# Kernel tuning notes

Measured on AMD Instinct MI355X. Metric: run time of the kernel, lower is better.

Reference implementation:

```python
import jax, jax.numpy as jnp
import numpy as np

N, E = 20000, 5000
IN_FT, OUT_FT = 128, 128
DENSITY = 0.01  # fraction of nonzeros in the incidence matrix


def setup_inputs() -> dict:
    key = jax.random.key(0)
    kx, kh, kw, kb = jax.random.split(key, 4)
    X = jax.random.normal(kx, (N, IN_FT), dtype=jnp.float32)
    H = (jax.random.uniform(kh, (N, E)) < DENSITY).astype(jnp.float32)
    # xavier_normal_ with gain=0.01
    xav_std = 0.01 * np.sqrt(2.0 / (IN_FT + OUT_FT))
    weight_trans = jax.random.normal(kw, (IN_FT, OUT_FT), dtype=jnp.float32) * xav_std
    bias = jax.random.normal(kb, (OUT_FT,), dtype=jnp.float32) * 0.01
    return {"X": X, "H": H, "weight_trans": weight_trans, "bias": bias}


def reference(X, H, weight_trans, bias):
    # X: [N, in_ft], H: [N, E] incidence
    Xw = X @ weight_trans                      # [N, out_ft]
    DV = jnp.sum(H, axis=1) + 1e-12            # node degrees, [N]
    DE = jnp.sum(H, axis=0) + 1e-12            # hyperedge degrees, [E]
    # G = diag(1/DV) @ H @ diag(1/DE) @ H^T applied to Xw, computed in the
    # efficient order without materializing the NxN matrix G:
    M = H.T @ Xw                               # [E, out_ft]
    M = M / DE[:, None]                        # diag(1/DE) scaling
    out = H @ M                                # [N, out_ft]
    out = out / DV[:, None]                    # diag(1/DV) scaling
    out = out + bias
    return jax.nn.relu(out)
```

## Files before the change

### kernel.cpp

```cpp
#include <hip/hip_runtime.h>
#include <hip/hip_bf16.h>

typedef unsigned long long u64;

#define N_NODES 20000
#define N_EDGES 5000
#define FT 128
#define NT 20
#define NRG 313
#define ROW_U64 80
#define COL_U64 320
#define MAX_DEG 320

__global__ __launch_bounds__(256) void x_to_bf16(
    const float2* __restrict__ X2, __hip_bfloat162* __restrict__ Xb2) {
  int i = blockIdx.x * 256 + threadIdx.x;
  Xb2[i] = __float22bfloat162_rn(X2[i]);
}

__global__ __launch_bounds__(64) void scan_bitmask(
    const float4* __restrict__ H4,
    u64* __restrict__ Hbt,
    u64* __restrict__ HbtT) {
  const int lane = threadIdx.x;
  const int t  = blockIdx.x % NT;
  const int rg = blockIdx.x / NT;
  const int r0 = rg * 64;
  const int rows = min(64, N_NODES - r0);
  const int idx4 = t * 64 + lane;
  const bool lv = idx4 < 1250;

  u64 m0 = 0, m1 = 0, m2 = 0, m3 = 0;
  for (int kb = 0; kb < rows; kb += 8) {
    float4 vv[8];
#pragma unroll
    for (int k = 0; k < 8; ++k) vv[k] = make_float4(0.f, 0.f, 0.f, 0.f);
    if (lv) {
      const float4* bp = H4 + (size_t)(r0 + kb) * 1250 + idx4;
#pragma unroll
      for (int k = 0; k < 8; ++k) vv[k] = bp[(size_t)k * 1250];
    }
#pragma unroll
    for (int k = 0; k < 8; ++k) {
      u64 b0 = __ballot(vv[k].x != 0.f);
      u64 b1 = __ballot(vv[k].y != 0.f);
      u64 b2 = __ballot(vv[k].z != 0.f);
      u64 b3 = __ballot(vv[k].w != 0.f);
      const bool keep = (lane == kb + k);
      m0 = keep ? b0 : m0;  m1 = keep ? b1 : m1;
      m2 = keep ? b2 : m2;  m3 = keep ? b3 : m3;
    }
  }
  if (lane < rows) {
    u64* hp = Hbt + (size_t)(r0 + lane) * ROW_U64 + t * 4;
    hp[0] = m0; hp[1] = m1; hp[2] = m2; hp[3] = m3;
  }
  u64 t0 = 0, t1 = 0, t2 = 0, t3 = 0;
  for (int l = 0; l < 64; ++l) {
    u64 c0 = __ballot((m0 >> l) & 1ull);
    u64 c1 = __ballot((m1 >> l) & 1ull);
    u64 c2 = __ballot((m2 >> l) & 1ull);
    u64 c3 = __ballot((m3 >> l) & 1ull);
    const bool keep = (lane == l);
    t0 = keep ? c0 : t0;  t1 = keep ? c1 : t1;
    t2 = keep ? c2 : t2;  t3 = keep ? c3 : t3;
  }
  const int c = t * 256 + 4 * lane;
  HbtT[(size_t)(c + 0) * COL_U64 + rg] = t0;
  HbtT[(size_t)(c + 1) * COL_U64 + rg] = t1;
  HbtT[(size_t)(c + 2) * COL_U64 + rg] = t2;
  HbtT[(size_t)(c + 3) * COL_U64 + rg] = t3;
}

__global__ __launch_bounds__(256) void edge_gather(
    const __hip_bfloat162* __restrict__ Xb2,
    const u64* __restrict__ HbtT,
    float2* __restrict__ P2, int* __restrict__ de) {
  __shared__ int sidx[4][MAX_DEG];
  const int wid = threadIdx.x >> 6, lane = threadIdx.x & 63;
  const int e = blockIdx.x * 4 + wid;

  const u64* cb = HbtT + (size_t)e * COL_U64;
  u64 cm[5];
#pragma unroll
  for (int q = 0; q < 5; ++q) {
    int u = q * 64 + lane;
    cm[q] = (u < NRG) ? cb[u] : 0ull;
  }
  int cnt = 0;
#pragma unroll
  for (int q = 0; q < 5; ++q) cnt += __popcll(cm[q]);
  int off = cnt;
  for (int d = 1; d < 64; d <<= 1) {
    int v = __shfl_up(off, d);
    if (lane >= d) off += v;
  }
  int total = __shfl(off, 63);
  off -= cnt;
#pragma unroll
  for (int q = 0; q < 5; ++q) {
    u64 w = cm[q];
    int rbase = q * 4096 + lane * 64;
    while (w) {
      int b = __ffsll(w) - 1;
      w &= w - 1;
      if (off < MAX_DEG) sidx[wid][off] = rbase + b;
      ++off;
    }
  }
  __builtin_amdgcn_s_waitcnt(0);
  int tt = min(total, MAX_DEG);

  float sx = 0.f, sy = 0.f;
  int g = 0;
  for (; g + 16 <= tt; g += 16) {
    int nn[16];
#pragma unroll
    for (int q = 0; q < 16; ++q) nn[q] = sidx[wid][g + q];
    float2 aa[16];
#pragma unroll
    for (int q = 0; q < 16; ++q) aa[q] = __bfloat1622float2(Xb2[nn[q] * 64 + lane]);
#pragma unroll
    for (int q = 0; q < 16; ++q) { sx += aa[q].x; sy += aa[q].y; }
  }
  for (; g < tt; ++g) {
    float2 a = __bfloat1622float2(Xb2[sidx[wid][g] * 64 + lane]);
    sx += a.x; sy += a.y;
  }
  P2[e * 64 + lane] = make_float2(sx, sy);
  if (lane == 0) de[e] = total;
}

__global__ __launch_bounds__(256) void gemm_M(
    const float* __restrict__ P, const float* __restrict__ W,
    const int* __restrict__ de, float* __restrict__ M) {
  int f = threadIdx.x & (FT - 1);
  int half = threadIdx.x >> 7;
  int base = blockIdx.x * 16 + half * 8;
#pragma unroll
  for (int g = 0; g < 8; g += 4) {
    int e = base + g;
    if (e >= N_EDGES) break;
    const float* p0 = P + (e + 0) * FT;
    const float* p1 = P + (e + 1) * FT;
    const float* p2 = P + (e + 2) * FT;
    const float* p3 = P + (e + 3) * FT;
    float a0 = 0.f, a1 = 0.f, a2 = 0.f, a3 = 0.f;
#pragma unroll 4
    for (int k = 0; k < FT; ++k) {
      float w = W[k * FT + f];
      a0 += p0[k] * w; a1 += p1[k] * w; a2 += p2[k] * w; a3 += p3[k] * w;
    }
    M[(e + 0) * FT + f] = a0 / ((float)de[e + 0] + 1e-12f);
    M[(e + 1) * FT + f] = a1 / ((float)de[e + 1] + 1e-12f);
    M[(e + 2) * FT + f] = a2 / ((float)de[e + 2] + 1e-12f);
    M[(e + 3) * FT + f] = a3 / ((float)de[e + 3] + 1e-12f);
  }
}

__global__ __launch_bounds__(256) void row_apply(
    const u64* __restrict__ Hbt,
    const float2* __restrict__ M2, const float2* __restrict__ bias2,
    float2* __restrict__ out2) {
  const int wid = threadIdx.x >> 6, lane = threadIdx.x & 63;
  const int n = blockIdx.x * 4 + wid;
  u64 m_lo = Hbt[(size_t)n * ROW_U64 + lane];
  u64 m_hi = (lane < ROW_U64 - 64) ? Hbt[(size_t)n * ROW_U64 + 64 + lane] : 0ull;
  float sx = 0.f, sy = 0.f;
  int dv = 0;
  for (int vp = 0; vp < ROW_U64; ++vp) {
    u64 mp = (vp < 64) ? __shfl(m_lo, vp) : __shfl(m_hi, vp - 64);
    if (mp == 0ull) continue;
    dv += __popcll(mp);
    int ebase = (vp >> 2) * 256 + (vp & 3);
    while (mp) {
      int b0 = __ffsll(mp) - 1; mp &= mp - 1;
      if (mp) {
        int b1 = __ffsll(mp) - 1; mp &= mp - 1;
        float2 u = M2[(size_t)(ebase + 4 * b0) * 64 + lane];
        float2 w = M2[(size_t)(ebase + 4 * b1) * 64 + lane];
        sx += u.x + w.x; sy += u.y + w.y;
      } else {
        float2 u = M2[(size_t)(ebase + 4 * b0) * 64 + lane];
        sx += u.x; sy += u.y;
      }
    }
  }
  float inv = 1.f / ((float)dv + 1e-12f);
  float2 bb = bias2[lane];
  float2 o;
  o.x = fmaxf(fmaf(sx, inv, bb.x), 0.f);
  o.y = fmaxf(fmaf(sy, inv, bb.y), 0.f);
  out2[(size_t)n * 64 + lane] = o;
}

extern "C" void kernel_launch(void* const* d_in, const int* in_sizes, int n_in,
                              void* d_out, int out_size, void* d_ws, size_t ws_size,
                              hipStream_t stream) {
  const float* X    = (const float*)d_in[0];
  const float* H    = (const float*)d_in[1];
  const float* W    = (const float*)d_in[2];
  const float* bias = (const float*)d_in[3];
  float* out = (float*)d_out;

  int* ws = (int*)d_ws;
  u64* Hbt             = (u64*)ws;
  u64* HbtT            = (u64*)(ws + 3200000);
  __hip_bfloat162* Xb2 = (__hip_bfloat162*)(ws + 6476800);
  float* P             = (float*)(ws + 7756800);
  int* de              = ws + 8396800;
  float* M             = (float*)(ws + 8401920);

  x_to_bf16   <<<5000, 256, 0, stream>>>((const float2*)X, Xb2);
  scan_bitmask<<<NRG * NT, 64, 0, stream>>>((const float4*)H, Hbt, HbtT);
  edge_gather <<<1250, 256, 0, stream>>>(Xb2, HbtT, (float2*)P, de);
  gemm_M      <<<(N_EDGES + 15) / 16, 256, 0, stream>>>(P, W, de, M);
  row_apply   <<<5000, 256, 0, stream>>>(Hbt, (const float2*)M,
                                         (const float2*)bias, (float2*)out);
}
```

Baseline: 674.0 us.

## Double-buffer H scan, split bitmask transpose, and compact row_apply edge list

The H scan kernel now packs four waves per block and double-buffers its float4 loads so the ballots on one batch of rows overlap the loads for the next. The bit transpose moves into a separate kernel, and its HbtT output is laid out row-group-major so the stores coalesce, at the cost of strided reads in edge_gather. row_apply first builds a compacted list of incident edge indices in shared memory via a prefix scan and then gathers M rows in unrolled batches of eight, replacing the per-word shuffle loop. The change adds an extra launch and a hard cap of 128 edges per node.

```diff
diff --git a/kernel.cpp b/kernel.cpp
--- a/kernel.cpp
+++ b/kernel.cpp
@@ -9,8 +9,9 @@
 #define NT 20
 #define NRG 313
 #define ROW_U64 80
-#define COL_U64 320
+#define COL_STRIDE 5120
 #define MAX_DEG 320
+#define MAX_NDEG 128
 
 __global__ __launch_bounds__(256) void x_to_bf16(
     const float2* __restrict__ X2, __hip_bfloat162* __restrict__ Xb2) {
@@ -18,58 +19,89 @@
   Xb2[i] = __float22bfloat162_rn(X2[i]);
 }
 
-__global__ __launch_bounds__(64) void scan_bitmask(
-    const float4* __restrict__ H4,
-    u64* __restrict__ Hbt,
-    u64* __restrict__ HbtT) {
-  const int lane = threadIdx.x;
-  const int t  = blockIdx.x % NT;
-  const int rg = blockIdx.x / NT;
+#define LOADB(dst, kb0) do {                                                   \
+    _Pragma("unroll")                                                          \
+    for (int k_ = 0; k_ < 8; ++k_) dst[k_] = make_float4(0.f, 0.f, 0.f, 0.f); \
+    if (lv) {                                                                  \
+      _Pragma("unroll")                                                        \
+      for (int k_ = 0; k_ < 8; ++k_)                                           \
+        dst[k_] = bp[(size_t)((kb0) + k_) * 1250];                             \
+    }                                                                          \
+  } while (0)
+
+#define PROCB(src, kb0) do {                                                   \
+    _Pragma("unroll")                                                          \
+    for (int k_ = 0; k_ < 8; ++k_) {                                           \
+      u64 b0_ = __ballot(src[k_].x != 0.f);                                    \
+      u64 b1_ = __ballot(src[k_].y != 0.f);                                    \
+      u64 b2_ = __ballot(src[k_].z != 0.f);                                    \
+      u64 b3_ = __ballot(src[k_].w != 0.f);                                    \
+      const bool keep_ = (lane == (kb0) + k_);                                 \
+      m0 = keep_ ? b0_ : m0;  m1 = keep_ ? b1_ : m1;                           \
+      m2 = keep_ ? b2_ : m2;  m3 = keep_ ? b3_ : m3;                           \
+    }                                                                          \
+  } while (0)
+
+__global__ __launch_bounds__(256) void scan_bitmask(
+    const float4* __restrict__ H4, u64* __restrict__ Hbt) {
+  const int wid = threadIdx.x >> 6, lane = threadIdx.x & 63;
+  const int gw = blockIdx.x * 4 + wid;
+  const int t = gw % NT, rg = gw / NT;
   const int r0 = rg * 64;
   const int rows = min(64, N_NODES - r0);
   const int idx4 = t * 64 + lane;
   const bool lv = idx4 < 1250;
+  const float4* bp = H4 + (size_t)r0 * 1250 + idx4;
 
   u64 m0 = 0, m1 = 0, m2 = 0, m3 = 0;
-  for (int kb = 0; kb < rows; kb += 8) {
-    float4 vv[8];
-#pragma unroll
-    for (int k = 0; k < 8; ++k) vv[k] = make_float4(0.f, 0.f, 0.f, 0.f);
-    if (lv) {
-      const float4* bp = H4 + (size_t)(r0 + kb) * 1250 + idx4;
-#pragma unroll
-      for (int k = 0; k < 8; ++k) vv[k] = bp[(size_t)k * 1250];
-    }
-#pragma unroll
-    for (int k = 0; k < 8; ++k) {
-      u64 b0 = __ballot(vv[k].x != 0.f);
-      u64 b1 = __ballot(vv[k].y != 0.f);
-      u64 b2 = __ballot(vv[k].z != 0.f);
-      u64 b3 = __ballot(vv[k].w != 0.f);
-      const bool keep = (lane == kb + k);
-      m0 = keep ? b0 : m0;  m1 = keep ? b1 : m1;
-      m2 = keep ? b2 : m2;  m3 = keep ? b3 : m3;
-    }
+  float4 a[8], b[8];
+  LOADB(a, 0);
+  if (rows == 64) {
+#pragma unroll
+    for (int kb = 0; kb < 64; kb += 16) {
+      LOADB(b, kb + 8);
+      PROCB(a, kb);
+      if (kb + 16 < 64) LOADB(a, kb + 16);
+      PROCB(b, kb + 8);
+    }
+  } else {
+    LOADB(b, 8);
+    PROCB(a, 0);
+    LOADB(a, 16);
+    PROCB(b, 8);
+    LOADB(b, 24);
+    PROCB(a, 16);
+    PROCB(b, 24);
   }
   if (lane < rows) {
     u64* hp = Hbt + (size_t)(r0 + lane) * ROW_U64 + t * 4;
     hp[0] = m0; hp[1] = m1; hp[2] = m2; hp[3] = m3;
   }
+}
+
+__global__ __launch_bounds__(256) void transpose_bm(
+    const u64* __restrict__ Hbt, u64* __restrict__ HbtT) {
+  const int wid = threadIdx.x >> 6, lane = threadIdx.x & 63;
+  const int gw = blockIdx.x * 4 + wid;
+  const int t = gw % NT, rg = gw / NT;
+  const int r = rg * 64 + lane;
+  u64 w0 = 0, w1 = 0, w2 = 0, w3 = 0;
+  if (r < N_NODES) {
+    const u64* hp = Hbt + (size_t)r * ROW_U64 + t * 4;
+    w0 = hp[0]; w1 = hp[1]; w2 = hp[2]; w3 = hp[3];
+  }
   u64 t0 = 0, t1 = 0, t2 = 0, t3 = 0;
   for (int l = 0; l < 64; ++l) {
-    u64 c0 = __ballot((m0 >> l) & 1ull);
-    u64 c1 = __ballot((m1 >> l) & 1ull);
-    u64 c2 = __ballot((m2 >> l) & 1ull);
-    u64 c3 = __ballot((m3 >> l) & 1ull);
+    u64 c0 = __ballot((w0 >> l) & 1ull);
+    u64 c1 = __ballot((w1 >> l) & 1ull);
+    u64 c2 = __ballot((w2 >> l) & 1ull);
+    u64 c3 = __ballot((w3 >> l) & 1ull);
     const bool keep = (lane == l);
     t0 = keep ? c0 : t0;  t1 = keep ? c1 : t1;
     t2 = keep ? c2 : t2;  t3 = keep ? c3 : t3;
   }
-  const int c = t * 256 + 4 * lane;
-  HbtT[(size_t)(c + 0) * COL_U64 + rg] = t0;
-  HbtT[(size_t)(c + 1) * COL_U64 + rg] = t1;
-  HbtT[(size_t)(c + 2) * COL_U64 + rg] = t2;
-  HbtT[(size_t)(c + 3) * COL_U64 + rg] = t3;
+  u64* op = HbtT + (size_t)rg * COL_STRIDE + t * 256 + 4 * lane;
+  op[0] = t0; op[1] = t1; op[2] = t2; op[3] = t3;
 }
 
 __global__ __launch_bounds__(256) void edge_gather(
@@ -80,12 +112,11 @@
   const int wid = threadIdx.x >> 6, lane = threadIdx.x & 63;
   const int e = blockIdx.x * 4 + wid;
 
-  const u64* cb = HbtT + (size_t)e * COL_U64;
   u64 cm[5];
 #pragma unroll
   for (int q = 0; q < 5; ++q) {
     int u = q * 64 + lane;
-    cm[q] = (u < NRG) ? cb[u] : 0ull;
+    cm[q] = (u < NRG) ? HbtT[(size_t)u * COL_STRIDE + e] : 0ull;
   }
   int cnt = 0;
 #pragma unroll
@@ -124,8 +155,8 @@
     for (int q = 0; q < 16; ++q) { sx += aa[q].x; sy += aa[q].y; }
   }
   for (; g < tt; ++g) {
-    float2 a = __bfloat1622float2(Xb2[sidx[wid][g] * 64 + lane]);
-    sx += a.x; sy += a.y;
+    float2 a2 = __bfloat1622float2(Xb2[sidx[wid][g] * 64 + lane]);
+    sx += a2.x; sy += a2.y;
   }
   P2[e * 64 + lane] = make_float2(sx, sy);
   if (lane == 0) de[e] = total;
@@ -162,31 +193,57 @@
     const u64* __restrict__ Hbt,
     const float2* __restrict__ M2, const float2* __restrict__ bias2,
     float2* __restrict__ out2) {
+  __shared__ int eidx[4][MAX_NDEG];
   const int wid = threadIdx.x >> 6, lane = threadIdx.x & 63;
   const int n = blockIdx.x * 4 + wid;
-  u64 m_lo = Hbt[(size_t)n * ROW_U64 + lane];
-  u64 m_hi = (lane < ROW_U64 - 64) ? Hbt[(size_t)n * ROW_U64 + 64 + lane] : 0ull;
+  const u64* hp = Hbt + (size_t)n * ROW_U64;
+  u64 mlo = hp[lane];
+  u64 mhi = (lane < ROW_U64 - 64) ? hp[64 + lane] : 0ull;
+  int cnt = __popcll(mlo) + __popcll(mhi);
+  int off = cnt;
+  for (int d = 1; d < 64; d <<= 1) {
+    int v = __shfl_up(off, d);
+    if (lane >= d) off += v;
+  }
+  int total = __shfl(off, 63);
+  off -= cnt;
+  {
+    int eb = (lane >> 2) * 256 + (lane & 3);
+    u64 w = mlo;
+    while (w) {
+      int b = __ffsll(w) - 1; w &= w - 1;
+      if (off < MAX_NDEG) eidx[wid][off] = eb + 4 * b;
+      ++off;
+    }
+    int vp = 64 + lane;
+    eb = (vp >> 2) * 256 + (vp & 3);
+    w = mhi;
+    while (w) {
+      int b = __ffsll(w) - 1; w &= w - 1;
+      if (off < MAX_NDEG) eidx[wid][off] = eb + 4 * b;
+      ++off;
+    }
+  }
+  __builtin_amdgcn_s_waitcnt(0);
+  int tt = min(total, MAX_NDEG);
+
   float sx = 0.f, sy = 0.f;
-  int dv = 0;
-  for (int vp = 0; vp < ROW_U64; ++vp) {
-    u64 mp = (vp < 64) ? __shfl(m_lo, vp) : __shfl(m_hi, vp - 64);
-    if (mp == 0ull) continue;
-    dv += __popcll(mp);
-    int ebase = (vp >> 2) * 256 + (vp & 3);
-    while (mp) {
-      int b0 = __ffsll(mp) - 1; mp &= mp - 1;
-      if (mp) {
-        int b1 = __ffsll(mp) - 1; mp &= mp - 1;
-        float2 u = M2[(size_t)(ebase + 4 * b0) * 64 + lane];
-        float2 w = M2[(size_t)(ebase + 4 * b1) * 64 + lane];
-        sx += u.x + w.x; sy += u.y + w.y;
-      } else {
-        float2 u = M2[(size_t)(ebase + 4 * b0) * 64 + lane];
-        sx += u.x; sy += u.y;
-      }
-    }
-  }
-  float inv = 1.f / ((float)dv + 1e-12f);
+  int g = 0;
+  for (; g + 8 <= tt; g += 8) {
+    int ee[8];
+#pragma unroll
+    for (int q = 0; q < 8; ++q) ee[q] = eidx[wid][g + q];
+    float2 vv[8];
+#pragma unroll
+    for (int q = 0; q < 8; ++q) vv[q] = M2[(size_t)ee[q] * 64 + lane];
+#pragma unroll
+    for (int q = 0; q < 8; ++q) { sx += vv[q].x; sy += vv[q].y; }
+  }
+  for (; g < tt; ++g) {
+    float2 v = M2[(size_t)eidx[wid][g] * 64 + lane];
+    sx += v.x; sy += v.y;
+  }
+  float inv = 1.f / ((float)total + 1e-12f);
   float2 bb = bias2[lane];
   float2 o;
   o.x = fmaxf(fmaf(sx, inv, bb.x), 0.f);
@@ -212,9 +269,10 @@
   float* M             = (float*)(ws + 8401920);
 
   x_to_bf16   <<<5000, 256, 0, stream>>>((const float2*)X, Xb2);
-  scan_bitmask<<<NRG * NT, 64, 0, stream>>>((const float4*)H, Hbt, HbtT);
+  scan_bitmask<<<1565, 256, 0, stream>>>((const float4*)H, Hbt);
+  transpose_bm<<<1565, 256, 0, stream>>>(Hbt, HbtT);
   edge_gather <<<1250, 256, 0, stream>>>(Xb2, HbtT, (float2*)P, de);
-  gemm_M      <<<(N_EDGES + 15) / 16, 256, 0, stream>>>(P, W, de, M);
+  gemm_M      <<<313, 256, 0, stream>>>(P, W, de, M);
   row_apply   <<<5000, 256, 0, stream>>>(Hbt, (const float2*)M,
                                          (const float2*)bias, (float2*)out);
 }
```

New measurement: 665.1 us. Within noise of the previous version (-1.3%).
